# Performance work log

Hardware: AMD Instinct MI355X
Metric: run time of the kernel (lower is better)

The kernel has to match this reference:

```python
import jax, jax.numpy as jnp
import numpy as np

IN_DIM, ATT_DIM, OUT_DIM, NH = 1024, 64, 64, 16
ATT_BIAS = 0.5


def setup_inputs() -> dict:
    key = jax.random.key(0)
    ks = jax.random.split(key, 11)
    B, S = 2, 2048
    s_in = 1.0 / np.sqrt(IN_DIM)
    s_o = 1.0 / np.sqrt(NH * OUT_DIM)
    return {
        "q": jax.random.normal(ks[0], (B, S, IN_DIM), jnp.float32),
        "k": jax.random.normal(ks[1], (B, S, IN_DIM), jnp.float32),
        "v": jax.random.normal(ks[2], (B, S, IN_DIM), jnp.float32),
        "Wq": jax.random.uniform(ks[3], (IN_DIM, NH * ATT_DIM), jnp.float32, -s_in, s_in),
        "bq": jax.random.uniform(ks[4], (NH * ATT_DIM,), jnp.float32, -s_in, s_in),
        "Wk": jax.random.uniform(ks[5], (IN_DIM, NH * ATT_DIM), jnp.float32, -s_in, s_in),
        "bk": jax.random.uniform(ks[6], (NH * ATT_DIM,), jnp.float32, -s_in, s_in),
        "Wv": jax.random.uniform(ks[7], (IN_DIM, NH * OUT_DIM), jnp.float32, -s_in, s_in),
        "bv": jax.random.uniform(ks[8], (NH * OUT_DIM,), jnp.float32, -s_in, s_in),
        "Wo": jax.random.uniform(ks[9], (NH * OUT_DIM, OUT_DIM), jnp.float32, -s_o, s_o),
        "bo": jax.random.uniform(ks[10], (OUT_DIM,), jnp.float32, -s_o, s_o),
    }


def reference(q, k, v, Wq, bq, Wk, bk, Wv, bv, Wo, bo):
    B, S, _ = q.shape
    scale = ATT_DIM ** -0.5
    # projections -> [B, H, S, d]
    qh = (q @ Wq + bq).reshape(B, S, NH, ATT_DIM).transpose(0, 2, 1, 3)
    kh = (k @ Wk + bk).reshape(B, S, NH, ATT_DIM).transpose(0, 2, 1, 3)
    vh = (v @ Wv + bv).reshape(B, S, NH, OUT_DIM).transpose(0, 2, 1, 3)
    # sigmoid-biased scores then softmax over keys
    scores = jnp.einsum("bhqd,bhkd->bhqk", qh * scale, kh)
    scores = jax.nn.sigmoid(scores) - ATT_BIAS
    attn = jax.nn.softmax(scores, axis=-1)
    out = jnp.einsum("bhqk,bhkd->bhqd", attn, vh)  # dropout p=0 -> identity
    out = out.transpose(0, 2, 1, 3).reshape(B, S, NH * OUT_DIM)
    return out @ Wo + bo
```

## Files before the change

### kernel.cpp

```cpp
#include <hip/hip_runtime.h>
#include <hip/hip_bf16.h>
#include <stdint.h>

typedef __bf16 bf16x8 __attribute__((ext_vector_type(8)));
typedef float  f32x4  __attribute__((ext_vector_type(4)));
typedef short  short4v __attribute__((ext_vector_type(4)));

__device__ __forceinline__ unsigned short f2bf(float f) {
  union { float f; unsigned u; } x; x.f = f;
  unsigned r = x.u + 0x7fffu + ((x.u >> 16) & 1u);
  return (unsigned short)(r >> 16);
}

__device__ __forceinline__ unsigned pack_rne(float a, float b) {
  unsigned ua = __float_as_uint(a), ub = __float_as_uint(b);
  ua = ua + 0x7fffu + ((ua >> 16) & 1u);
  ub = ub + 0x7fffu + ((ub >> 16) & 1u);
  return __builtin_amdgcn_perm(ub, ua, 0x07060302);
}

__device__ __forceinline__ f32x4 mfma16(short4v a, short4v b, f32x4 c) {
#if __has_builtin(__builtin_amdgcn_mfma_f32_16x16x16bf16_1k)
  return __builtin_amdgcn_mfma_f32_16x16x16bf16_1k(a, b, c, 0, 0, 0);
#else
  f32x4 d;
  asm volatile("v_mfma_f32_16x16x16_bf16 %0, %1, %2, %3\n\ts_nop 7\n\ts_nop 7"
               : "=v"(d) : "v"(a), "v"(b), "v"(c));
  return d;
#endif
}

__device__ __forceinline__ float fast_exp2(float p) {
#if __has_builtin(__builtin_amdgcn_exp2f)
  return __builtin_amdgcn_exp2f(p);
#else
  return exp2f(p);
#endif
}

__device__ __forceinline__ void gll16(const void* g, void* l) {
  __builtin_amdgcn_global_load_lds((const __attribute__((address_space(1))) void*)g,
                                   (__attribute__((address_space(3))) void*)l, 16, 0, 0);
}

__global__ __launch_bounds__(256) void k_prep(
    const float* __restrict__ q, const float* __restrict__ k, const float* __restrict__ v,
    const float* __restrict__ Wq, const float* __restrict__ Wk,
    const float* __restrict__ Wv, const float* __restrict__ Wo,
    const float* __restrict__ bo,
    unsigned short* __restrict__ qb, unsigned short* __restrict__ kb,
    unsigned short* __restrict__ vb,
    unsigned short* __restrict__ Wqt, unsigned short* __restrict__ Wkt,
    unsigned short* __restrict__ Wvt, unsigned short* __restrict__ Wot,
    float* __restrict__ out) {
  __shared__ float tt[32][33];
  int b = blockIdx.x, tid = threadIdx.x;
  if (b < 12288) {
    int z = b >> 12;
    const float* src = z == 0 ? q : z == 1 ? k : v;
    unsigned short* dst = z == 0 ? qb : z == 1 ? kb : vb;
    size_t i = (size_t)(b & 4095) * 256 + tid;
    float4 f = ((const float4*)src)[i];
    ushort4 o;
    o.x = f2bf(f.x); o.y = f2bf(f.y); o.z = f2bf(f.z); o.w = f2bf(f.w);
    ((ushort4*)dst)[i] = o;
  } else if (b < 15424) {
    int t = b - 12288;
    const float* W; unsigned short* Wt; int C, c0, r0;
    if (t < 3072) {
      int z = t >> 10;
      W = z == 0 ? Wq : z == 1 ? Wk : Wv;
      Wt = z == 0 ? Wqt : z == 1 ? Wkt : Wvt;
      C = 1024; int tile = t & 1023;
      c0 = (tile & 31) * 32; r0 = (tile >> 5) * 32;
    } else {
      int t2 = t - 3072;
      W = Wo; Wt = Wot; C = 64;
      c0 = (t2 & 1) * 32; r0 = (t2 >> 1) * 32;
    }
    int tx = tid & 31, ty = tid >> 5;
    #pragma unroll
    for (int i = 0; i < 32; i += 8)
      tt[ty + i][tx] = W[(size_t)(r0 + ty + i) * C + c0 + tx];
    __syncthreads();
    #pragma unroll
    for (int i = 0; i < 32; i += 8)
      Wt[(size_t)(c0 + ty + i) * 1024 + r0 + tx] = f2bf(tt[tx][ty + i]);
  } else {
    int t3 = b - 15424;
    int i = t3 * 1024 + tid * 4;
    float4 bv4 = *(const float4*)(bo + (i & 63));
    *(float4*)(out + i) = bv4;
  }
}

__global__ __launch_bounds__(256, 3) void k_proj(
    const unsigned short* __restrict__ qb, const unsigned short* __restrict__ kb,
    const unsigned short* __restrict__ vb,
    const unsigned short* __restrict__ Wqt, const unsigned short* __restrict__ Wkt,
    const unsigned short* __restrict__ Wvt,
    const float* __restrict__ bq, const float* __restrict__ bk, const float* __restrict__ bv,
    unsigned short* __restrict__ qh, unsigned short* __restrict__ kh,
    unsigned short* __restrict__ vht) {
  int z = blockIdx.z;
  const unsigned short* A  = z == 0 ? qb  : z == 1 ? kb  : vb;
  const unsigned short* Bt = z == 0 ? Wqt : z == 1 ? Wkt : Wvt;
  const float* bias = z == 0 ? bq : z == 1 ? bk : bv;

  int m0 = blockIdx.y * 128;
  int n0 = blockIdx.x * 128;

  __shared__ __attribute__((aligned(16))) unsigned short As[128 * 64];
  __shared__ __attribute__((aligned(16))) unsigned short Bs[128 * 64];

  int tid = threadIdx.x;
  int w = tid >> 6, lane = tid & 63;
  int wm = w >> 1, wn = w & 1;
  int lr = lane & 15, lk = lane >> 4;

  f32x4 acc[4][4] = {};

  for (int k0 = 0; k0 < 1024; k0 += 64) {
    #pragma unroll
    for (int i = 0; i < 4; ++i) {
      int cc = i * 256 + tid;
      int r = cc >> 3;
      int j = (cc & 7) ^ (r & 7);
      gll16(A + (size_t)(m0 + r) * 1024 + k0 + j * 8, As + (size_t)(i * 256 + w * 64) * 8);
    }
    #pragma unroll
    for (int i = 0; i < 4; ++i) {
      int cc = i * 256 + tid;
      int r = cc >> 3;
      int j = (cc & 7) ^ (r & 7);
      gll16(Bt + (size_t)(n0 + r) * 1024 + k0 + j * 8, Bs + (size_t)(i * 256 + w * 64) * 8);
    }
    __syncthreads();
    #pragma unroll
    for (int ks = 0; ks < 2; ++ks) {
      bf16x8 af[4], bfr[4];
      #pragma unroll
      for (int mt = 0; mt < 4; ++mt) {
        int r = wm * 64 + mt * 16 + lr;
        af[mt] = *(const bf16x8*)(As + r * 64 + ((ks * 4 + lk) ^ (r & 7)) * 8);
      }
      #pragma unroll
      for (int nt = 0; nt < 4; ++nt) {
        int r = wn * 64 + nt * 16 + lr;
        bfr[nt] = *(const bf16x8*)(Bs + r * 64 + ((ks * 4 + lk) ^ (r & 7)) * 8);
      }
      #pragma unroll
      for (int mt = 0; mt < 4; ++mt)
        #pragma unroll
        for (int nt = 0; nt < 4; ++nt)
          acc[mt][nt] = __builtin_amdgcn_mfma_f32_16x16x32_bf16(af[mt], bfr[nt], acc[mt][nt], 0, 0, 0);
    }
    __syncthreads();
  }

  #pragma unroll
  for (int nt = 0; nt < 4; ++nt) {
    int n = n0 + wn * 64 + nt * 16 + lr;
    float bv_ = bias[n];
    int h = n >> 6, d = n & 63;
    #pragma unroll
    for (int mt = 0; mt < 4; ++mt) {
      int mbase = m0 + wm * 64 + mt * 16 + lk * 4;
      int b = mbase >> 11, s = mbase & 2047;
      if (z == 2) {
        size_t o = ((size_t)(b * 16 + h) * 64 + d) * 2048 + s;
        ushort4 pk;
        pk.x = f2bf(acc[mt][nt][0] + bv_);
        pk.y = f2bf(acc[mt][nt][1] + bv_);
        pk.z = f2bf(acc[mt][nt][2] + bv_);
        pk.w = f2bf(acc[mt][nt][3] + bv_);
        *(ushort4*)(vht + o) = pk;
      } else {
        unsigned short* dst = (z == 0) ? qh : kh;
        float sc = (z == 0) ? 0.125f : 1.0f;
        #pragma unroll
        for (int rg = 0; rg < 4; ++rg) {
          float val = (acc[mt][nt][rg] + bv_) * sc;
          float pv = __shfl_xor(val, 1, 64);
          if ((lr & 1) == 0) {
            unsigned pkv = pack_rne(val, pv);
            *(unsigned*)(dst + ((size_t)(b * 16 + h) * 2048 + (s + rg)) * 64 + d) = pkv;
          }
        }
      }
    }
  }
}

__global__ __launch_bounds__(256, 2) void k_attn(
    const unsigned short* __restrict__ qh, const unsigned short* __restrict__ kh,
    const unsigned short* __restrict__ vht, unsigned short* __restrict__ attout) {
  int bh = blockIdx.y;
  int q0 = blockIdx.x * 128;
  const unsigned short* Q = qh + (size_t)bh * 2048 * 64;
  const unsigned short* Kg = kh + (size_t)bh * 2048 * 64;
  const unsigned short* Vg = vht + (size_t)bh * 64 * 2048;

  __shared__ __attribute__((aligned(16))) unsigned short KV[17408];
  __shared__ float lsum[128];

  int tid = threadIdx.x;
  int w = tid >> 6, lane = tid & 63;
  int wm = w >> 1, wn = w & 1;
  int c = lane & 15, qd = lane >> 4;

  bf16x8 qf[4][2];
  #pragma unroll
  for (int nt = 0; nt < 4; ++nt)
    #pragma unroll
    for (int ks = 0; ks < 2; ++ks)
      qf[nt][ks] = *(const bf16x8*)(Q + (size_t)(q0 + wn * 64 + nt * 16 + c) * 64 + ks * 32 + qd * 8);

  size_t kOff[2], vOff[2]; int lOff[2];
  #pragma unroll
  for (int i = 0; i < 2; ++i) {
    int cc = i * 256 + w * 64 + lane;
    int r = cc >> 3;
    int j = (cc & 7) ^ (r & 7);
    kOff[i] = (size_t)r * 64 + j * 8;
    vOff[i] = (size_t)r * 2048 + j * 8;
    lOff[i] = (i * 256 + w * 64) * 8;
  }

  #pragma unroll
  for (int i = 0; i < 2; ++i) {
    gll16(Kg + kOff[i], KV + lOff[i]);
    gll16(Vg + vOff[i], KV + 4096 + lOff[i]);
  }
  Kg += 4096; Vg += 64;

  int kfA[2][2], vfA[4][2];
  #pragma unroll
  for (int mt = 0; mt < 2; ++mt) {
    int r = wm * 32 + mt * 16 + c;
    #pragma unroll
    for (int ks = 0; ks < 2; ++ks)
      kfA[mt][ks] = r * 64 + ((ks * 4 + qd) ^ (r & 7)) * 8;
  }
  #pragma unroll
  for (int dt = 0; dt < 4; ++dt) {
    int r = dt * 16 + c;
    #pragma unroll
    for (int mt = 0; mt < 2; ++mt)
      vfA[dt][mt] = r * 64 + ((4 * wm + 2 * mt + (qd >> 1)) ^ (r & 7)) * 8 + (qd & 1) * 4;
  }

  const short one_bf = (short)0x3F80;
  short4v ones = {one_bf, one_bf, one_bf, one_bf};

  __syncthreads();

  f32x4 o[4][4] = {};
  f32x4 qacc[4] = {};

  for (int kt = 0; kt < 32; ++kt) {
    unsigned short* Kc = KV + (kt & 1) * 8192;
    unsigned short* Vc = Kc + 4096;
    if (kt + 1 < 32) {
      unsigned short* Kn = KV + ((kt & 1) ^ 1) * 8192;
      #pragma unroll
      for (int i = 0; i < 2; ++i) {
        gll16(Kg + kOff[i], Kn + lOff[i]);
        gll16(Vg + vOff[i], Kn + 4096 + lOff[i]);
      }
      Kg += 4096; Vg += 64;
    }

    f32x4 s[2][4] = {};
    #pragma unroll
    for (int ks = 0; ks < 2; ++ks) {
      bf16x8 kf[2];
      #pragma unroll
      for (int mt = 0; mt < 2; ++mt)
        kf[mt] = *(const bf16x8*)(Kc + kfA[mt][ks]);
      #pragma unroll
      for (int mt = 0; mt < 2; ++mt)
        #pragma unroll
        for (int nt = 0; nt < 4; ++nt)
          s[mt][nt] = __builtin_amdgcn_mfma_f32_16x16x32_bf16(kf[mt], qf[nt][ks], s[mt][nt], 0, 0, 0);
    }

    unsigned pk[2][4][2];
    #pragma unroll
    for (int mt = 0; mt < 2; ++mt)
      #pragma unroll
      for (int nt = 0; nt < 4; ++nt) {
        unsigned wu[4];
        #pragma unroll
        for (int rg = 0; rg < 4; ++rg) {
          float sv = __builtin_amdgcn_fmed3f(s[mt][nt][rg], -4.0f, 4.0f);
          float z = sv * sv;
          float p = fmaf(z, fmaf(z, fmaf(z, -3.9242863e-5f, 1.5674414e-3f),
                                  -2.6566200e-2f), 3.5838444e-1f) * sv;
          wu[rg] = __float_as_uint(fast_exp2(p));
        }
        pk[mt][nt][0] = __builtin_amdgcn_perm(wu[1], wu[0], 0x07060302);
        pk[mt][nt][1] = __builtin_amdgcn_perm(wu[3], wu[2], 0x07060302);
      }

    short4v vfr[4][2];
    #pragma unroll
    for (int dt = 0; dt < 4; ++dt)
      #pragma unroll
      for (int mt = 0; mt < 2; ++mt)
        vfr[dt][mt] = *(const short4v*)(Vc + vfA[dt][mt]);
    #pragma unroll
    for (int nt = 0; nt < 4; ++nt)
      #pragma unroll
      for (int mt = 0; mt < 2; ++mt) {
        union { unsigned u[2]; short4v s4; } bb;
        bb.u[0] = pk[mt][nt][0];
        bb.u[1] = pk[mt][nt][1];
        qacc[nt] = mfma16(ones, bb.s4, qacc[nt]);
        #pragma unroll
        for (int dt = 0; dt < 4; ++dt)
          o[dt][nt] = mfma16(vfr[dt][mt], bb.s4, o[dt][nt]);
      }
    __syncthreads();
  }

  float* Ored = (float*)KV;
  if (wm == 1) {
    #pragma unroll
    for (int nt = 0; nt < 4; ++nt) {
      int ql = wn * 64 + nt * 16 + c;
      #pragma unroll
      for (int dt = 0; dt < 4; ++dt)
        *(f32x4*)(Ored + ql * 68 + dt * 16 + qd * 4) = o[dt][nt];
      if (qd == 0) lsum[ql] = qacc[nt][0];
    }
  }
  __syncthreads();
  if (wm == 0) {
    int b = bh >> 4, h = bh & 15;
    #pragma unroll
    for (int nt = 0; nt < 4; ++nt) {
      int ql = wn * 64 + nt * 16 + c;
      float inv = __builtin_amdgcn_rcpf(qacc[nt][0] + lsum[ql]);
      size_t rowoff = ((size_t)(b * 2048 + q0 + ql)) * 1024 + h * 64;
      #pragma unroll
      for (int dt = 0; dt < 4; ++dt) {
        f32x4 r = *(const f32x4*)(Ored + ql * 68 + dt * 16 + qd * 4);
        f32x4 t = o[dt][nt];
        uint2 pko;
        pko.x = pack_rne((t[0] + r[0]) * inv, (t[1] + r[1]) * inv);
        pko.y = pack_rne((t[2] + r[2]) * inv, (t[3] + r[3]) * inv);
        *(uint2*)(attout + rowoff + dt * 16 + qd * 4) = pko;
      }
    }
  }
}

__global__ __launch_bounds__(256) void k_oproj(
    const unsigned short* __restrict__ attout, const unsigned short* __restrict__ Wot,
    float* __restrict__ out) {
  int m0 = blockIdx.x * 64;
  int kbase = blockIdx.y * 256;
  __shared__ __attribute__((aligned(16))) unsigned short As[64 * 32];
  __shared__ __attribute__((aligned(16))) unsigned short Bs[64 * 32];
  int tid = threadIdx.x;
  int w = tid >> 6, lane = tid & 63;
  int lr = lane & 15, lk = lane >> 4;

  f32x4 acc[4] = {};

  for (int k0 = kbase; k0 < kbase + 256; k0 += 32) {
    {
      int cc = tid;
      int r = cc >> 2;
      int j = (cc & 3) ^ ((r >> 1) & 3);
      gll16(attout + (size_t)(m0 + r) * 1024 + k0 + j * 8, As + (size_t)(w * 64) * 8);
      gll16(Wot + (size_t)r * 1024 + k0 + j * 8, Bs + (size_t)(w * 64) * 8);
    }
    __syncthreads();
    bf16x8 af, bfr[4];
    {
      int r = w * 16 + lr;
      af = *(const bf16x8*)(As + r * 32 + ((lk ^ ((r >> 1) & 3))) * 8);
    }
    #pragma unroll
    for (int nt = 0; nt < 4; ++nt) {
      int r = nt * 16 + lr;
      bfr[nt] = *(const bf16x8*)(Bs + r * 32 + ((lk ^ ((r >> 1) & 3))) * 8);
    }
    #pragma unroll
    for (int nt = 0; nt < 4; ++nt)
      acc[nt] = __builtin_amdgcn_mfma_f32_16x16x32_bf16(af, bfr[nt], acc[nt], 0, 0, 0);
    __syncthreads();
  }
  #pragma unroll
  for (int nt = 0; nt < 4; ++nt) {
    int n = nt * 16 + lr;
    #pragma unroll
    for (int rg = 0; rg < 4; ++rg) {
      int m = m0 + w * 16 + lk * 4 + rg;
      atomicAdd(&out[(size_t)m * 64 + n], acc[nt][rg]);
    }
  }
}

extern "C" void kernel_launch(void* const* d_in, const int* in_sizes, int n_in,
                              void* d_out, int out_size, void* d_ws, size_t ws_size,
                              hipStream_t stream) {
  const float* q  = (const float*)d_in[0];
  const float* k  = (const float*)d_in[1];
  const float* v  = (const float*)d_in[2];
  const float* Wq = (const float*)d_in[3];
  const float* bq = (const float*)d_in[4];
  const float* Wk = (const float*)d_in[5];
  const float* bk = (const float*)d_in[6];
  const float* Wv = (const float*)d_in[7];
  const float* bv = (const float*)d_in[8];
  const float* Wo = (const float*)d_in[9];
  const float* bo = (const float*)d_in[10];
  float* out = (float*)d_out;

  char* ws = (char*)d_ws;
  const size_t MB = 1024 * 1024;
  unsigned short* qb  = (unsigned short*)(ws + 0 * MB);
  unsigned short* kb  = (unsigned short*)(ws + 8 * MB);
  unsigned short* vb  = (unsigned short*)(ws + 16 * MB);
  unsigned short* Wqt = (unsigned short*)(ws + 24 * MB);
  unsigned short* Wkt = (unsigned short*)(ws + 26 * MB);
  unsigned short* Wvt = (unsigned short*)(ws + 28 * MB);
  unsigned short* Wot = (unsigned short*)(ws + 30 * MB);
  unsigned short* qh  = (unsigned short*)(ws + 32 * MB);
  unsigned short* kh  = (unsigned short*)(ws + 40 * MB);
  unsigned short* vht = (unsigned short*)(ws + 48 * MB);
  unsigned short* att = (unsigned short*)(ws + 56 * MB);

  k_prep<<<dim3(15680), dim3(256), 0, stream>>>(q, k, v, Wq, Wk, Wv, Wo, bo,
                                                qb, kb, vb, Wqt, Wkt, Wvt, Wot, out);
  k_proj<<<dim3(8, 32, 3), dim3(256), 0, stream>>>(qb, kb, vb, Wqt, Wkt, Wvt,
                                                   bq, bk, bv, qh, kh, vht);
  k_attn<<<dim3(16, 32), dim3(256), 0, stream>>>(qh, kh, vht, att);
  k_oproj<<<dim3(64, 4), dim3(256), 0, stream>>>(att, Wot, out);
}
```

Baseline: 219.4 us.

## Halve attention query tile, split keys across four waves, sum denominators in VALU

The attention kernel now handles 64 queries per block instead of 128, doubling the grid to 1024 blocks and raising the occupancy hint to 4 blocks per SM. Each of the four waves takes a 16-key slice of every key tile for all 64 queries. The partial outputs are then combined with a two-level LDS reduction. The softmax denominator is now summed from the packed bf16 weights with scalar adds, cross-lane shuffles and LDS atomics, which replaces the extra MFMA against a ones vector. This aims to improve occupancy and cut MFMA work, but each K/V tile is loaded twice as often and the epilogue needs extra barriers.

```diff
diff --git a/kernel.cpp b/kernel.cpp
--- a/kernel.cpp
+++ b/kernel.cpp
@@ -192,21 +192,20 @@
   }
 }
 
-__global__ __launch_bounds__(256, 2) void k_attn(
+__global__ __launch_bounds__(256, 4) void k_attn(
     const unsigned short* __restrict__ qh, const unsigned short* __restrict__ kh,
     const unsigned short* __restrict__ vht, unsigned short* __restrict__ attout) {
   int bh = blockIdx.y;
-  int q0 = blockIdx.x * 128;
+  int q0 = blockIdx.x * 64;
   const unsigned short* Q = qh + (size_t)bh * 2048 * 64;
   const unsigned short* Kg = kh + (size_t)bh * 2048 * 64;
   const unsigned short* Vg = vht + (size_t)bh * 64 * 2048;
 
-  __shared__ __attribute__((aligned(16))) unsigned short KV[17408];
-  __shared__ float lsum[128];
+  __shared__ __attribute__((aligned(16))) unsigned short KV[17664];
+  __shared__ float lsum[64];
 
   int tid = threadIdx.x;
   int w = tid >> 6, lane = tid & 63;
-  int wm = w >> 1, wn = w & 1;
   int c = lane & 15, qd = lane >> 4;
 
   bf16x8 qf[4][2];
@@ -214,7 +213,7 @@
   for (int nt = 0; nt < 4; ++nt)
     #pragma unroll
     for (int ks = 0; ks < 2; ++ks)
-      qf[nt][ks] = *(const bf16x8*)(Q + (size_t)(q0 + wn * 64 + nt * 16 + c) * 64 + ks * 32 + qd * 8);
+      qf[nt][ks] = *(const bf16x8*)(Q + (size_t)(q0 + nt * 16 + c) * 64 + ks * 32 + qd * 8);
 
   size_t kOff[2], vOff[2]; int lOff[2];
   #pragma unroll
@@ -234,29 +233,25 @@
   }
   Kg += 4096; Vg += 64;
 
-  int kfA[2][2], vfA[4][2];
-  #pragma unroll
-  for (int mt = 0; mt < 2; ++mt) {
-    int r = wm * 32 + mt * 16 + c;
+  int kfA[2];
+  {
+    int r = w * 16 + c;
     #pragma unroll
     for (int ks = 0; ks < 2; ++ks)
-      kfA[mt][ks] = r * 64 + ((ks * 4 + qd) ^ (r & 7)) * 8;
-  }
+      kfA[ks] = r * 64 + ((ks * 4 + qd) ^ (r & 7)) * 8;
+  }
+  int vfA[4];
   #pragma unroll
   for (int dt = 0; dt < 4; ++dt) {
     int r = dt * 16 + c;
-    #pragma unroll
-    for (int mt = 0; mt < 2; ++mt)
-      vfA[dt][mt] = r * 64 + ((4 * wm + 2 * mt + (qd >> 1)) ^ (r & 7)) * 8 + (qd & 1) * 4;
-  }
-
-  const short one_bf = (short)0x3F80;
-  short4v ones = {one_bf, one_bf, one_bf, one_bf};
-
+    vfA[dt] = r * 64 + ((w * 2 + (qd >> 1)) ^ (r & 7)) * 8 + (qd & 1) * 4;
+  }
+
+  if (tid < 64) lsum[tid] = 0.0f;
   __syncthreads();
 
   f32x4 o[4][4] = {};
-  f32x4 qacc[4] = {};
+  float qs[4] = {0.f, 0.f, 0.f, 0.f};
 
   for (int kt = 0; kt < 32; ++kt) {
     unsigned short* Kc = KV + (kt & 1) * 8192;
@@ -271,81 +266,99 @@
       Kg += 4096; Vg += 64;
     }
 
-    f32x4 s[2][4] = {};
+    f32x4 s[4] = {};
     #pragma unroll
     for (int ks = 0; ks < 2; ++ks) {
-      bf16x8 kf[2];
-      #pragma unroll
-      for (int mt = 0; mt < 2; ++mt)
-        kf[mt] = *(const bf16x8*)(Kc + kfA[mt][ks]);
-      #pragma unroll
-      for (int mt = 0; mt < 2; ++mt)
-        #pragma unroll
-        for (int nt = 0; nt < 4; ++nt)
-          s[mt][nt] = __builtin_amdgcn_mfma_f32_16x16x32_bf16(kf[mt], qf[nt][ks], s[mt][nt], 0, 0, 0);
-    }
-
-    unsigned pk[2][4][2];
-    #pragma unroll
-    for (int mt = 0; mt < 2; ++mt)
-      #pragma unroll
-      for (int nt = 0; nt < 4; ++nt) {
-        unsigned wu[4];
-        #pragma unroll
-        for (int rg = 0; rg < 4; ++rg) {
-          float sv = __builtin_amdgcn_fmed3f(s[mt][nt][rg], -4.0f, 4.0f);
-          float z = sv * sv;
-          float p = fmaf(z, fmaf(z, fmaf(z, -3.9242863e-5f, 1.5674414e-3f),
-                                  -2.6566200e-2f), 3.5838444e-1f) * sv;
-          wu[rg] = __float_as_uint(fast_exp2(p));
-        }
-        pk[mt][nt][0] = __builtin_amdgcn_perm(wu[1], wu[0], 0x07060302);
-        pk[mt][nt][1] = __builtin_amdgcn_perm(wu[3], wu[2], 0x07060302);
-      }
-
-    short4v vfr[4][2];
+      bf16x8 kf = *(const bf16x8*)(Kc + kfA[ks]);
+      #pragma unroll
+      for (int nt = 0; nt < 4; ++nt)
+        s[nt] = __builtin_amdgcn_mfma_f32_16x16x32_bf16(kf, qf[nt][ks], s[nt], 0, 0, 0);
+    }
+
+    unsigned pk[4][2];
+    #pragma unroll
+    for (int nt = 0; nt < 4; ++nt) {
+      unsigned wu[4];
+      #pragma unroll
+      for (int rg = 0; rg < 4; ++rg) {
+        float sv = __builtin_amdgcn_fmed3f(s[nt][rg], -4.0f, 4.0f);
+        float z = sv * sv;
+        float p = fmaf(z, fmaf(z, fmaf(z, -3.9242863e-5f, 1.5674414e-3f),
+                                -2.6566200e-2f), 3.5838444e-1f) * sv;
+        wu[rg] = __float_as_uint(fast_exp2(p));
+      }
+      unsigned p0 = __builtin_amdgcn_perm(wu[1], wu[0], 0x07060302);
+      unsigned p1 = __builtin_amdgcn_perm(wu[3], wu[2], 0x07060302);
+      pk[nt][0] = p0; pk[nt][1] = p1;
+      qs[nt] += (__uint_as_float(p0 << 16) + __uint_as_float(p0 & 0xffff0000u))
+              + (__uint_as_float(p1 << 16) + __uint_as_float(p1 & 0xffff0000u));
+    }
+
+    short4v vfr[4];
     #pragma unroll
     for (int dt = 0; dt < 4; ++dt)
-      #pragma unroll
-      for (int mt = 0; mt < 2; ++mt)
-        vfr[dt][mt] = *(const short4v*)(Vc + vfA[dt][mt]);
+      vfr[dt] = *(const short4v*)(Vc + vfA[dt]);
+    #pragma unroll
+    for (int nt = 0; nt < 4; ++nt) {
+      union { unsigned u[2]; short4v s4; } bb;
+      bb.u[0] = pk[nt][0];
+      bb.u[1] = pk[nt][1];
+      #pragma unroll
+      for (int dt = 0; dt < 4; ++dt)
+        o[dt][nt] = mfma16(vfr[dt], bb.s4, o[dt][nt]);
+    }
+    __syncthreads();
+  }
+
+  #pragma unroll
+  for (int nt = 0; nt < 4; ++nt) {
+    qs[nt] += __shfl_xor(qs[nt], 16, 64);
+    qs[nt] += __shfl_xor(qs[nt], 32, 64);
+  }
+  if (qd == 0) {
     #pragma unroll
     for (int nt = 0; nt < 4; ++nt)
-      #pragma unroll
-      for (int mt = 0; mt < 2; ++mt) {
-        union { unsigned u[2]; short4v s4; } bb;
-        bb.u[0] = pk[mt][nt][0];
-        bb.u[1] = pk[mt][nt][1];
-        qacc[nt] = mfma16(ones, bb.s4, qacc[nt]);
-        #pragma unroll
-        for (int dt = 0; dt < 4; ++dt)
-          o[dt][nt] = mfma16(vfr[dt][mt], bb.s4, o[dt][nt]);
-      }
-    __syncthreads();
-  }
-
-  float* Ored = (float*)KV;
-  if (wm == 1) {
+      atomicAdd(&lsum[nt * 16 + c], qs[nt]);
+  }
+
+  float* R0 = (float*)KV;
+  float* R1 = R0 + 4352;
+  if (w == 1 || w == 3) {
+    float* R = (w == 1) ? R0 : R1;
+    #pragma unroll
+    for (int nt = 0; nt < 4; ++nt)
+      #pragma unroll
+      for (int dt = 0; dt < 4; ++dt)
+        *(f32x4*)(R + (nt * 16 + c) * 68 + dt * 16 + qd * 4) = o[dt][nt];
+  }
+  __syncthreads();
+  if (w == 0 || w == 2) {
+    float* R = (w == 0) ? R0 : R1;
+    #pragma unroll
+    for (int nt = 0; nt < 4; ++nt)
+      #pragma unroll
+      for (int dt = 0; dt < 4; ++dt)
+        o[dt][nt] += *(const f32x4*)(R + (nt * 16 + c) * 68 + dt * 16 + qd * 4);
+  }
+  __syncthreads();
+  if (w == 2) {
+    #pragma unroll
+    for (int nt = 0; nt < 4; ++nt)
+      #pragma unroll
+      for (int dt = 0; dt < 4; ++dt)
+        *(f32x4*)(R0 + (nt * 16 + c) * 68 + dt * 16 + qd * 4) = o[dt][nt];
+  }
+  __syncthreads();
+  if (w == 0) {
+    int b = bh >> 4, h = bh & 15;
     #pragma unroll
     for (int nt = 0; nt < 4; ++nt) {
-      int ql = wn * 64 + nt * 16 + c;
-      #pragma unroll
-      for (int dt = 0; dt < 4; ++dt)
-        *(f32x4*)(Ored + ql * 68 + dt * 16 + qd * 4) = o[dt][nt];
-      if (qd == 0) lsum[ql] = qacc[nt][0];
-    }
-  }
-  __syncthreads();
-  if (wm == 0) {
-    int b = bh >> 4, h = bh & 15;
-    #pragma unroll
-    for (int nt = 0; nt < 4; ++nt) {
-      int ql = wn * 64 + nt * 16 + c;
-      float inv = __builtin_amdgcn_rcpf(qacc[nt][0] + lsum[ql]);
+      int ql = nt * 16 + c;
+      float inv = __builtin_amdgcn_rcpf(lsum[ql]);
       size_t rowoff = ((size_t)(b * 2048 + q0 + ql)) * 1024 + h * 64;
       #pragma unroll
       for (int dt = 0; dt < 4; ++dt) {
-        f32x4 r = *(const f32x4*)(Ored + ql * 68 + dt * 16 + qd * 4);
+        f32x4 r = *(const f32x4*)(R0 + ql * 68 + dt * 16 + qd * 4);
         f32x4 t = o[dt][nt];
         uint2 pko;
         pko.x = pack_rne((t[0] + r[0]) * inv, (t[1] + r[1]) * inv);
@@ -438,6 +451,6 @@
                                                 qb, kb, vb, Wqt, Wkt, Wvt, Wot, out);
   k_proj<<<dim3(8, 32, 3), dim3(256), 0, stream>>>(qb, kb, vb, Wqt, Wkt, Wvt,
                                                    bq, bk, bv, qh, kh, vht);
-  k_attn<<<dim3(16, 32), dim3(256), 0, stream>>>(qh, kh, vht, att);
+  k_attn<<<dim3(32, 32), dim3(256), 0, stream>>>(qh, kh, vht, att);
   k_oproj<<<dim3(64, 4), dim3(256), 0, stream>>>(att, Wot, out);
 }
```

New measurement: 255.6 us. 1.16x slower.

## Widen attention blocks to 8 waves with 128-key tiles and staged reduction

Applied to the files above, without the earlier changes.

The attention kernel now runs 512 threads per block. Each block loads 128-key K/V tiles, which halves the number of outer iterations, and the four key-split wave rows each take a 32-key slice. Partial outputs are reduced into wave row 0 through three staged shared-memory exchanges, and row sums are combined with shared atomics. The intent is more parallelism per block and fewer loop-level barriers, at the cost of more shared memory, extra reduction syncs, and possibly lower occupancy with the 512,3 launch bound.

```diff
diff --git a/kernel.cpp b/kernel.cpp
--- a/kernel.cpp
+++ b/kernel.cpp
@@ -192,7 +192,7 @@
   }
 }
 
-__global__ __launch_bounds__(256, 2) void k_attn(
+__global__ __launch_bounds__(512, 3) void k_attn(
     const unsigned short* __restrict__ qh, const unsigned short* __restrict__ kh,
     const unsigned short* __restrict__ vht, unsigned short* __restrict__ attout) {
   int bh = blockIdx.y;
@@ -201,7 +201,7 @@
   const unsigned short* Kg = kh + (size_t)bh * 2048 * 64;
   const unsigned short* Vg = vht + (size_t)bh * 64 * 2048;
 
-  __shared__ __attribute__((aligned(16))) unsigned short KV[17408];
+  __shared__ __attribute__((aligned(16))) unsigned short KV[32768];
   __shared__ float lsum[128];
 
   int tid = threadIdx.x;
@@ -219,20 +219,20 @@
   size_t kOff[2], vOff[2]; int lOff[2];
   #pragma unroll
   for (int i = 0; i < 2; ++i) {
-    int cc = i * 256 + w * 64 + lane;
-    int r = cc >> 3;
-    int j = (cc & 7) ^ (r & 7);
-    kOff[i] = (size_t)r * 64 + j * 8;
-    vOff[i] = (size_t)r * 2048 + j * 8;
-    lOff[i] = (i * 256 + w * 64) * 8;
+    int cc = i * 512 + w * 64 + lane;
+    int rk = cc >> 3, jk = (cc & 7) ^ (rk & 7);
+    int rv = cc >> 4, jv = (cc & 15) ^ (rv & 15);
+    kOff[i] = (size_t)rk * 64 + jk * 8;
+    vOff[i] = (size_t)rv * 2048 + jv * 8;
+    lOff[i] = cc * 8;
   }
 
   #pragma unroll
   for (int i = 0; i < 2; ++i) {
     gll16(Kg + kOff[i], KV + lOff[i]);
-    gll16(Vg + vOff[i], KV + 4096 + lOff[i]);
-  }
-  Kg += 4096; Vg += 64;
+    gll16(Vg + vOff[i], KV + 8192 + lOff[i]);
+  }
+  Kg += 8192; Vg += 128;
 
   int kfA[2][2], vfA[4][2];
   #pragma unroll
@@ -247,28 +247,29 @@
     int r = dt * 16 + c;
     #pragma unroll
     for (int mt = 0; mt < 2; ++mt)
-      vfA[dt][mt] = r * 64 + ((4 * wm + 2 * mt + (qd >> 1)) ^ (r & 7)) * 8 + (qd & 1) * 4;
+      vfA[dt][mt] = r * 128 + (((wm * 4 + mt * 2 + (qd >> 1))) ^ (r & 15)) * 8 + (qd & 1) * 4;
   }
 
   const short one_bf = (short)0x3F80;
   short4v ones = {one_bf, one_bf, one_bf, one_bf};
 
+  if (tid < 128) lsum[tid] = 0.0f;
   __syncthreads();
 
   f32x4 o[4][4] = {};
   f32x4 qacc[4] = {};
 
-  for (int kt = 0; kt < 32; ++kt) {
-    unsigned short* Kc = KV + (kt & 1) * 8192;
-    unsigned short* Vc = Kc + 4096;
-    if (kt + 1 < 32) {
-      unsigned short* Kn = KV + ((kt & 1) ^ 1) * 8192;
+  for (int kt = 0; kt < 16; ++kt) {
+    unsigned short* Kc = KV + (kt & 1) * 16384;
+    unsigned short* Vc = Kc + 8192;
+    if (kt + 1 < 16) {
+      unsigned short* Kn = KV + ((kt & 1) ^ 1) * 16384;
       #pragma unroll
       for (int i = 0; i < 2; ++i) {
         gll16(Kg + kOff[i], Kn + lOff[i]);
-        gll16(Vg + vOff[i], Kn + 4096 + lOff[i]);
-      }
-      Kg += 4096; Vg += 64;
+        gll16(Vg + vOff[i], Kn + 8192 + lOff[i]);
+      }
+      Kg += 8192; Vg += 128;
     }
 
     f32x4 s[2][4] = {};
@@ -324,32 +325,50 @@
     __syncthreads();
   }
 
-  float* Ored = (float*)KV;
-  if (wm == 1) {
+  if (qd == 0) {
+    #pragma unroll
+    for (int nt = 0; nt < 4; ++nt)
+      atomicAdd(&lsum[wn * 64 + nt * 16 + c], qacc[nt][0]);
+  }
+
+  float* R0 = (float*)KV;
+  #pragma unroll
+  for (int src = 1; src <= 3; ++src) {
+    if (wm == src) {
+      #pragma unroll
+      for (int nt = 0; nt < 4; ++nt) {
+        int ql = wn * 64 + nt * 16 + c;
+        #pragma unroll
+        for (int dt = 0; dt < 4; ++dt)
+          *(f32x4*)(R0 + ql * 66 + dt * 16 + qd * 4) = o[dt][nt];
+      }
+    }
+    __syncthreads();
+    if (wm == 0) {
+      #pragma unroll
+      for (int nt = 0; nt < 4; ++nt) {
+        int ql = wn * 64 + nt * 16 + c;
+        #pragma unroll
+        for (int dt = 0; dt < 4; ++dt)
+          o[dt][nt] += *(const f32x4*)(R0 + ql * 66 + dt * 16 + qd * 4);
+      }
+    }
+    __syncthreads();
+  }
+
+  if (wm == 0) {
+    int b = bh >> 4, h = bh & 15;
     #pragma unroll
     for (int nt = 0; nt < 4; ++nt) {
       int ql = wn * 64 + nt * 16 + c;
-      #pragma unroll
-      for (int dt = 0; dt < 4; ++dt)
-        *(f32x4*)(Ored + ql * 68 + dt * 16 + qd * 4) = o[dt][nt];
-      if (qd == 0) lsum[ql] = qacc[nt][0];
-    }
-  }
-  __syncthreads();
-  if (wm == 0) {
-    int b = bh >> 4, h = bh & 15;
-    #pragma unroll
-    for (int nt = 0; nt < 4; ++nt) {
-      int ql = wn * 64 + nt * 16 + c;
-      float inv = __builtin_amdgcn_rcpf(qacc[nt][0] + lsum[ql]);
+      float inv = __builtin_amdgcn_rcpf(lsum[ql]);
       size_t rowoff = ((size_t)(b * 2048 + q0 + ql)) * 1024 + h * 64;
       #pragma unroll
       for (int dt = 0; dt < 4; ++dt) {
-        f32x4 r = *(const f32x4*)(Ored + ql * 68 + dt * 16 + qd * 4);
         f32x4 t = o[dt][nt];
         uint2 pko;
-        pko.x = pack_rne((t[0] + r[0]) * inv, (t[1] + r[1]) * inv);
-        pko.y = pack_rne((t[2] + r[2]) * inv, (t[3] + r[3]) * inv);
+        pko.x = pack_rne(t[0] * inv, t[1] * inv);
+        pko.y = pack_rne(t[2] * inv, t[3] * inv);
         *(uint2*)(attout + rowoff + dt * 16 + qd * 4) = pko;
       }
     }
@@ -438,6 +457,6 @@
                                                 qb, kb, vb, Wqt, Wkt, Wvt, Wot, out);
   k_proj<<<dim3(8, 32, 3), dim3(256), 0, stream>>>(qb, kb, vb, Wqt, Wkt, Wvt,
                                                    bq, bk, bv, qh, kh, vht);
-  k_attn<<<dim3(16, 32), dim3(256), 0, stream>>>(qh, kh, vht, att);
+  k_attn<<<dim3(16, 32), dim3(512), 0, stream>>>(qh, kh, vht, att);
   k_oproj<<<dim3(64, 4), dim3(256), 0, stream>>>(att, Wot, out);
 }
```

After: 241.5 us. 1.1x slower.

## Double-buffer projection GEMM loads and widen split-K in output projection

Applied to the files above, without the earlier changes.

The projection GEMM now stages 32-wide K tiles into two alternating LDS buffers, issuing the next tile's async global-to-LDS loads before computing on the current one, with one barrier per step. Fragment addresses are precomputed outside the loop. Separately, the output projection grid grows from 4 to 16 K-splits, each covering 64 instead of 256 of K, to raise parallelism. The finer split adds more atomic or partial-sum traffic, and the narrower K tile halves work per barrier.

```diff
diff --git a/kernel.cpp b/kernel.cpp
--- a/kernel.cpp
+++ b/kernel.cpp
@@ -103,58 +103,73 @@
     unsigned short* __restrict__ qh, unsigned short* __restrict__ kh,
     unsigned short* __restrict__ vht) {
   int z = blockIdx.z;
-  const unsigned short* A  = z == 0 ? qb  : z == 1 ? kb  : vb;
-  const unsigned short* Bt = z == 0 ? Wqt : z == 1 ? Wkt : Wvt;
+  const unsigned short* Ap = z == 0 ? qb  : z == 1 ? kb  : vb;
+  const unsigned short* Bp = z == 0 ? Wqt : z == 1 ? Wkt : Wvt;
   const float* bias = z == 0 ? bq : z == 1 ? bk : bv;
 
   int m0 = blockIdx.y * 128;
   int n0 = blockIdx.x * 128;
 
-  __shared__ __attribute__((aligned(16))) unsigned short As[128 * 64];
-  __shared__ __attribute__((aligned(16))) unsigned short Bs[128 * 64];
+  __shared__ __attribute__((aligned(16))) unsigned short LB[16384];
 
   int tid = threadIdx.x;
   int w = tid >> 6, lane = tid & 63;
   int wm = w >> 1, wn = w & 1;
   int lr = lane & 15, lk = lane >> 4;
 
+  size_t aOff[2], bOff[2]; int lA[2];
+  #pragma unroll
+  for (int i = 0; i < 2; ++i) {
+    int cc = i * 256 + tid;
+    int r = cc >> 2;
+    int j = (cc & 3) ^ ((r >> 1) & 3);
+    aOff[i] = (size_t)(m0 + r) * 1024 + j * 8;
+    bOff[i] = (size_t)(n0 + r) * 1024 + j * 8;
+    lA[i] = cc * 8;
+  }
+
+  int afA[4], bfA[4];
+  #pragma unroll
+  for (int mt = 0; mt < 4; ++mt) {
+    int r = wm * 64 + mt * 16 + lr;
+    afA[mt] = r * 32 + (lk ^ ((r >> 1) & 3)) * 8;
+  }
+  #pragma unroll
+  for (int nt = 0; nt < 4; ++nt) {
+    int r = wn * 64 + nt * 16 + lr;
+    bfA[nt] = r * 32 + (lk ^ ((r >> 1) & 3)) * 8;
+  }
+
   f32x4 acc[4][4] = {};
 
-  for (int k0 = 0; k0 < 1024; k0 += 64) {
-    #pragma unroll
-    for (int i = 0; i < 4; ++i) {
-      int cc = i * 256 + tid;
-      int r = cc >> 3;
-      int j = (cc & 7) ^ (r & 7);
-      gll16(A + (size_t)(m0 + r) * 1024 + k0 + j * 8, As + (size_t)(i * 256 + w * 64) * 8);
-    }
-    #pragma unroll
-    for (int i = 0; i < 4; ++i) {
-      int cc = i * 256 + tid;
-      int r = cc >> 3;
-      int j = (cc & 7) ^ (r & 7);
-      gll16(Bt + (size_t)(n0 + r) * 1024 + k0 + j * 8, Bs + (size_t)(i * 256 + w * 64) * 8);
-    }
-    __syncthreads();
-    #pragma unroll
-    for (int ks = 0; ks < 2; ++ks) {
-      bf16x8 af[4], bfr[4];
-      #pragma unroll
-      for (int mt = 0; mt < 4; ++mt) {
-        int r = wm * 64 + mt * 16 + lr;
-        af[mt] = *(const bf16x8*)(As + r * 64 + ((ks * 4 + lk) ^ (r & 7)) * 8);
-      }
-      #pragma unroll
-      for (int nt = 0; nt < 4; ++nt) {
-        int r = wn * 64 + nt * 16 + lr;
-        bfr[nt] = *(const bf16x8*)(Bs + r * 64 + ((ks * 4 + lk) ^ (r & 7)) * 8);
-      }
-      #pragma unroll
-      for (int mt = 0; mt < 4; ++mt)
-        #pragma unroll
-        for (int nt = 0; nt < 4; ++nt)
-          acc[mt][nt] = __builtin_amdgcn_mfma_f32_16x16x32_bf16(af[mt], bfr[nt], acc[mt][nt], 0, 0, 0);
-    }
+  #pragma unroll
+  for (int i = 0; i < 2; ++i) gll16(Ap + aOff[i], LB + lA[i]);
+  #pragma unroll
+  for (int i = 0; i < 2; ++i) gll16(Bp + bOff[i], LB + 4096 + lA[i]);
+  Ap += 32; Bp += 32;
+  __syncthreads();
+
+  for (int kt = 0; kt < 32; ++kt) {
+    unsigned short* As = LB + (kt & 1) * 8192;
+    unsigned short* Bs = As + 4096;
+    if (kt + 1 < 32) {
+      unsigned short* Ln = LB + ((kt & 1) ^ 1) * 8192;
+      #pragma unroll
+      for (int i = 0; i < 2; ++i) gll16(Ap + aOff[i], Ln + lA[i]);
+      #pragma unroll
+      for (int i = 0; i < 2; ++i) gll16(Bp + bOff[i], Ln + 4096 + lA[i]);
+      Ap += 32; Bp += 32;
+    }
+    bf16x8 af[4], bfr[4];
+    #pragma unroll
+    for (int mt = 0; mt < 4; ++mt) af[mt] = *(const bf16x8*)(As + afA[mt]);
+    #pragma unroll
+    for (int nt = 0; nt < 4; ++nt) bfr[nt] = *(const bf16x8*)(Bs + bfA[nt]);
+    #pragma unroll
+    for (int mt = 0; mt < 4; ++mt)
+      #pragma unroll
+      for (int nt = 0; nt < 4; ++nt)
+        acc[mt][nt] = __builtin_amdgcn_mfma_f32_16x16x32_bf16(af[mt], bfr[nt], acc[mt][nt], 0, 0, 0);
     __syncthreads();
   }
 
@@ -360,7 +375,7 @@
     const unsigned short* __restrict__ attout, const unsigned short* __restrict__ Wot,
     float* __restrict__ out) {
   int m0 = blockIdx.x * 64;
-  int kbase = blockIdx.y * 256;
+  int kbase = blockIdx.y * 64;
   __shared__ __attribute__((aligned(16))) unsigned short As[64 * 32];
   __shared__ __attribute__((aligned(16))) unsigned short Bs[64 * 32];
   int tid = threadIdx.x;
@@ -369,7 +384,7 @@
 
   f32x4 acc[4] = {};
 
-  for (int k0 = kbase; k0 < kbase + 256; k0 += 32) {
+  for (int k0 = kbase; k0 < kbase + 64; k0 += 32) {
     {
       int cc = tid;
       int r = cc >> 2;
@@ -439,5 +454,5 @@
   k_proj<<<dim3(8, 32, 3), dim3(256), 0, stream>>>(qb, kb, vb, Wqt, Wkt, Wvt,
                                                    bq, bk, bv, qh, kh, vht);
   k_attn<<<dim3(16, 32), dim3(256), 0, stream>>>(qh, kh, vht, att);
-  k_oproj<<<dim3(64, 4), dim3(256), 0, stream>>>(att, Wot, out);
-}
+  k_oproj<<<dim3(64, 16), dim3(256), 0, stream>>>(att, Wot, out);
+}
```

Measured after the change: 227.0 us. 3.5% more time.
